# Optimization experiments

Measured on AMD Instinct MI355X. Metric: run time of the kernel, lower is better.

Reference implementation:

```python
import jax, jax.numpy as jnp
import numpy as np

D_MODEL = 1024
NHEADS = 16
DIM_K = D_MODEL // NHEADS


def setup_inputs() -> dict:
    key = jax.random.key(0)
    ks = jax.random.split(key, 7)
    B, S = 4, 2048
    scale = 1.0 / np.sqrt(D_MODEL)
    return {
        "Q": jax.random.normal(ks[0], (B, S, D_MODEL), jnp.float32),
        "K": jax.random.normal(ks[1], (B, S, D_MODEL), jnp.float32),
        "V": jax.random.normal(ks[2], (B, S, D_MODEL), jnp.float32),
        "Wq": jax.random.normal(ks[3], (D_MODEL, D_MODEL), jnp.float32) * scale,
        "Wk": jax.random.normal(ks[4], (D_MODEL, D_MODEL), jnp.float32) * scale,
        "Wv": jax.random.normal(ks[5], (D_MODEL, D_MODEL), jnp.float32) * scale,
        "Wo": jax.random.normal(ks[6], (D_MODEL, D_MODEL), jnp.float32) * scale,
    }


def _split(x):
    # [B,S,D] -> [B,H,S,dk]
    B, S, _ = x.shape
    return x.reshape(B, S, NHEADS, DIM_K).transpose(0, 2, 1, 3)


def reference(Q, K, V, Wq, Wk, Wv, Wo):
    # nn.Linear(x) = x @ W.T; weights stored torch-style [out, in]
    q = _split(Q @ Wq.T)  # [B,H,S,dk]
    k = _split(K @ Wk.T)
    v = _split(V @ Wv.T)
    scores = jnp.einsum("bhsd,bhtd->bhst", q, k) / jnp.sqrt(jnp.float32(DIM_K))
    attn = jax.nn.softmax(scores, axis=-1)
    out = jnp.einsum("bhst,bhtd->bhsd", attn, v)  # [B,H,S,dk]
    B, H, S, dk = out.shape
    out = out.transpose(0, 2, 1, 3).reshape(B, S, H * dk)
    return out @ Wo.T
```

## Files before the change

kernel.cpp:

```cpp
#include <hip/hip_runtime.h>
#include <math.h>
#include <stdint.h>

#define D_MODEL 1024
#define NHEADS  16
#define DK      64
#define BATCH   4
#define SEQ     2048
#define MROWS   (BATCH * SEQ)
#define TENS    ((size_t)MROWS * D_MODEL)
#define WELT    ((size_t)D_MODEL * D_MODEL)

typedef __attribute__((ext_vector_type(8))) _Float16 f16x8;
typedef __attribute__((ext_vector_type(2))) __fp16 h16x2;
typedef __attribute__((ext_vector_type(4))) float f32x4;
typedef __attribute__((ext_vector_type(8))) unsigned short us8;
typedef __attribute__((ext_vector_type(4))) unsigned short us4;

__device__ __forceinline__ unsigned short f2h(float x) {
    _Float16 h = (_Float16)x;
    return __builtin_bit_cast(unsigned short, h);
}

#if __has_builtin(__builtin_amdgcn_exp2f)
__device__ __forceinline__ float fexp2(float x) { return __builtin_amdgcn_exp2f(x); }
#else
__device__ __forceinline__ float fexp2(float x) { return exp2f(x); }
#endif

__device__ __forceinline__ void gld_lds16(const void* g, void* l) {
    __builtin_amdgcn_global_load_lds(
        (__attribute__((address_space(1))) void*)(uintptr_t)(g),
        (__attribute__((address_space(3))) void*)(unsigned)(uintptr_t)(l),
        16, 0, 0);
}

__global__ __launch_bounds__(256)
void convert_kernel(const float* __restrict__ q, const float* __restrict__ k,
                    const float* __restrict__ v, const float* __restrict__ wq,
                    const float* __restrict__ wk, const float* __restrict__ wv,
                    const float* __restrict__ wo, unsigned short* __restrict__ dst)
{
    const int seg = blockIdx.y;
    size_t i = ((size_t)blockIdx.x * 256 + threadIdx.x) * 4;
    const float* src;
    size_t doff, soff;
    if (seg < 3) {
        if (i >= TENS) return;
        src = (seg == 0) ? q : (seg == 1) ? k : v;
        soff = i;
        doff = (size_t)seg * TENS + i;
    } else {
        if (i >= 4 * WELT) return;
        const int widx = (int)(i >> 20);
        src = (widx == 0) ? wq : (widx == 1) ? wk : (widx == 2) ? wv : wo;
        soff = i & (WELT - 1);
        doff = 3 * TENS + i;
    }
    float4 f = *(const float4*)(src + soff);
    us4 o = { f2h(f.x), f2h(f.y), f2h(f.z), f2h(f.w) };
    *(us4*)(dst + doff) = o;
}

__device__ __forceinline__
void gemm_body(const unsigned short* __restrict__ A,
               const unsigned short* __restrict__ B,
               void* __restrict__ C, int N, int K, int omode,
               unsigned short* As, unsigned short* Bs)
{
    const int tid  = threadIdx.x;
    const int wave = tid >> 6;
    const int lane = tid & 63;
    const int g    = lane >> 4;
    const int m15  = lane & 15;
    const int bm   = blockIdx.x * 128;
    const int bn   = blockIdx.y * 128;

    const int srw = lane >> 3;
    const int lc  = (lane & 7) ^ srw;

    const int wr = (wave >> 1) * 64;
    const int wc = (wave & 1) * 64;

    f32x4 acc[4][4];
#pragma unroll
    for (int i = 0; i < 4; ++i)
#pragma unroll
        for (int j = 0; j < 4; ++j) acc[i][j] = (f32x4){0.f, 0.f, 0.f, 0.f};

    for (int k0 = 0; k0 < K; k0 += 64) {
        __syncthreads();
#pragma unroll
        for (int i = 0; i < 4; ++i) {
            const int rb = wave * 32 + i * 8;
            gld_lds16(A + (size_t)(bm + rb + srw) * K + k0 + lc * 8,
                      &As[rb * 64]);
            gld_lds16(B + (size_t)(bn + rb + srw) * K + k0 + lc * 8,
                      &Bs[rb * 64]);
        }
        __syncthreads();

#pragma unroll
        for (int t = 0; t < 2; ++t) {
            f16x8 af[4], bf[4];
#pragma unroll
            for (int i = 0; i < 4; ++i) {
                int row = wr + i * 16 + m15;
                int pc  = (4 * t + g) ^ (row & 7);
                af[i] = *(const f16x8*)&As[row * 64 + pc * 8];
            }
#pragma unroll
            for (int j = 0; j < 4; ++j) {
                int row = wc + j * 16 + m15;
                int pc  = (4 * t + g) ^ (row & 7);
                bf[j] = *(const f16x8*)&Bs[row * 64 + pc * 8];
            }
#pragma unroll
            for (int i = 0; i < 4; ++i)
#pragma unroll
                for (int j = 0; j < 4; ++j)
                    acc[i][j] = __builtin_amdgcn_mfma_f32_16x16x32_f16(
                        af[i], bf[j], acc[i][j], 0, 0, 0);
        }
    }

#pragma unroll
    for (int i = 0; i < 4; ++i) {
        const int gm0 = bm + wr + i * 16 + g * 4;
#pragma unroll
        for (int j = 0; j < 4; ++j) {
            const int gn = bn + wc + j * 16 + m15;
            if (omode == 0) {
#pragma unroll
                for (int r = 0; r < 4; ++r)
                    ((float*)C)[(size_t)(gm0 + r) * N + gn] = acc[i][j][r];
            } else if (omode == 1) {
#pragma unroll
                for (int r = 0; r < 4; ++r)
                    ((unsigned short*)C)[(size_t)(gm0 + r) * N + gn] = f2h(acc[i][j][r]);
            } else {
                const int b_ = gm0 >> 11, s_ = gm0 & 2047;
                const int h_ = gn >> 6,  d_ = gn & 63;
                us4 o = { f2h(acc[i][j][0]), f2h(acc[i][j][1]),
                          f2h(acc[i][j][2]), f2h(acc[i][j][3]) };
                *(us4*)((unsigned short*)C +
                        (((size_t)(b_ * NHEADS + h_) * 256 + (s_ >> 3)) * 64 + d_) * 8
                        + (s_ & 7)) = o;
            }
        }
    }
}

__global__ __launch_bounds__(256)
void proj3_kernel(const unsigned short* __restrict__ qb,
                  const unsigned short* __restrict__ kb,
                  const unsigned short* __restrict__ vb,
                  const unsigned short* __restrict__ wq,
                  const unsigned short* __restrict__ wk,
                  const unsigned short* __restrict__ wv,
                  unsigned short* __restrict__ qproj,
                  unsigned short* __restrict__ kproj,
                  unsigned short* __restrict__ vtw)
{
    __shared__ unsigned short As[128 * 64];
    __shared__ unsigned short Bs[128 * 64];
    const int z = blockIdx.z;
    const unsigned short* A = (z == 0) ? qb : (z == 1) ? kb : vb;
    const unsigned short* B = (z == 0) ? wq : (z == 1) ? wk : wv;
    void* C = (z == 0) ? (void*)qproj : (z == 1) ? (void*)kproj : (void*)vtw;
    gemm_body(A, B, C, D_MODEL, D_MODEL, (z == 2) ? 2 : 1, As, Bs);
}

__global__ __launch_bounds__(256)
void gemm_out_kernel(const unsigned short* __restrict__ A,
                     const unsigned short* __restrict__ B,
                     float* __restrict__ C)
{
    __shared__ unsigned short As[128 * 64];
    __shared__ unsigned short Bs[128 * 64];
    gemm_body(A, B, C, D_MODEL, D_MODEL, 0, As, Bs);
}

__global__ __launch_bounds__(256, 2)
void attn_kernel(const unsigned short* __restrict__ qp,
                 const unsigned short* __restrict__ kp,
                 const unsigned short* __restrict__ vt,
                 unsigned short* __restrict__ ao)
{
    __shared__ unsigned short Ks[2][64 * 64];
    __shared__ unsigned short VTs[2][64 * 64];
    __shared__ unsigned short Ps[4][16 * 72];

    const int tid = threadIdx.x;
    const int w = tid >> 6, lane = tid & 63;
    const int g = lane >> 4, m15 = lane & 15;
    const int qt = blockIdx.x, h = blockIdx.y, b = blockIdx.z;

    const int q0 = qt * 256 + w * 64;
    const size_t rowbase = (size_t)b * SEQ;

    const int srw = lane >> 3;
    const int lc  = (lane & 7) ^ srw;

    const _Float16 qscale = (_Float16)(0.125f * 1.4426950408889634f);
    f16x8 qf[4][2];
#pragma unroll
    for (int mi = 0; mi < 4; ++mi)
#pragma unroll
        for (int t = 0; t < 2; ++t) {
            f16x8 v = *(const f16x8*)(qp + (rowbase + q0 + mi * 16 + m15) * D_MODEL
                                      + h * DK + t * 32 + g * 8);
            qf[mi][t] = v * qscale;
        }

    const _Float16 one16 = (_Float16)1.f;
    const f16x8 onesf = { one16, one16, one16, one16, one16, one16, one16, one16 };

    float mrun[4] = {-INFINITY, -INFINITY, -INFINITY, -INFINITY};
    float lrun[4] = {0.f, 0.f, 0.f, 0.f};

    f32x4 accO[4][4];
#pragma unroll
    for (int mi = 0; mi < 4; ++mi)
#pragma unroll
        for (int i = 0; i < 4; ++i) accO[mi][i] = (f32x4){0.f, 0.f, 0.f, 0.f};

    const unsigned short* kbase = kp + rowbase * D_MODEL + h * DK;
    const unsigned short* vbase = vt + (size_t)(b * NHEADS + h) * DK * SEQ;

    auto stage = [&](int buf, int t) {
#pragma unroll
        for (int it = 0; it < 2; ++it) {
            const int rb = w * 16 + it * 8;
            gld_lds16(kbase + (size_t)(t * 64 + rb + srw) * D_MODEL + lc * 8,
                      &Ks[buf][rb * 64]);
            gld_lds16(vbase + ((size_t)(t * 8 + lc) * 64 + rb + srw) * 8,
                      &VTs[buf][rb * 64]);
        }
    };

    const int NT = SEQ / 64;
    stage(0, 0);
    __syncthreads();

    for (int kt = 0; kt < NT; ++kt) {
        const int cur = kt & 1;
        if (kt + 1 < NT) stage(cur ^ 1, kt + 1);

        f32x4 ST[4][4];
        __builtin_amdgcn_s_setprio(1);
#pragma unroll
        for (int km = 0; km < 4; ++km) {
            const int row = km * 16 + m15;
            f16x8 kf0 = *(const f16x8*)&Ks[cur][row * 64 + ((0 + g) ^ (row & 7)) * 8];
            f16x8 kf1 = *(const f16x8*)&Ks[cur][row * 64 + ((4 + g) ^ (row & 7)) * 8];
#pragma unroll
            for (int mi = 0; mi < 4; ++mi) {
                f32x4 z = (f32x4){0.f, 0.f, 0.f, 0.f};
                z = __builtin_amdgcn_mfma_f32_16x16x32_f16(kf0, qf[mi][0], z, 0, 0, 0);
                z = __builtin_amdgcn_mfma_f32_16x16x32_f16(kf1, qf[mi][1], z, 0, 0, 0);
                ST[km][mi] = z;
            }
        }
        __builtin_amdgcn_s_setprio(0);

        float scl[4];
        f16x8 pf[4][2];
#pragma unroll
        for (int mi = 0; mi < 4; ++mi) {
            float t0 = fmaxf(fmaxf(ST[0][mi][0], ST[0][mi][1]), ST[0][mi][2]);
            float t1 = fmaxf(fmaxf(ST[0][mi][3], ST[1][mi][0]), ST[1][mi][1]);
            float t2 = fmaxf(fmaxf(ST[1][mi][2], ST[1][mi][3]), ST[2][mi][0]);
            float t3 = fmaxf(fmaxf(ST[2][mi][1], ST[2][mi][2]), ST[2][mi][3]);
            float t4 = fmaxf(fmaxf(ST[3][mi][0], ST[3][mi][1]), ST[3][mi][2]);
            float u0 = fmaxf(fmaxf(t0, t1), t2);
            float u1 = fmaxf(fmaxf(t3, t4), ST[3][mi][3]);
            float mx = fmaxf(u0, u1);
            mx = fmaxf(mx, __shfl_xor(mx, 16));
            mx = fmaxf(mx, __shfl_xor(mx, 32));
            float mnew = fmaxf(mrun[mi], mx);
            scl[mi] = fexp2(mrun[mi] - mnew);
            mrun[mi] = mnew;
#pragma unroll
            for (int km = 0; km < 4; ++km) {
                float p0 = fexp2(ST[km][mi][0] - mnew);
                float p1 = fexp2(ST[km][mi][1] - mnew);
                float p2 = fexp2(ST[km][mi][2] - mnew);
                float p3 = fexp2(ST[km][mi][3] - mnew);
                h16x2 d0 = __builtin_amdgcn_cvt_pkrtz(p0, p1);
                h16x2 d1 = __builtin_amdgcn_cvt_pkrtz(p2, p3);
                uint2 wv = { __builtin_bit_cast(unsigned, d0),
                             __builtin_bit_cast(unsigned, d1) };
                *(uint2*)&Ps[w][m15 * 72 + km * 16 + g * 4] = wv;
            }
            pf[mi][0] = *(const f16x8*)&Ps[w][m15 * 72 + g * 8];
            pf[mi][1] = *(const f16x8*)&Ps[w][m15 * 72 + 32 + g * 8];
            f32x4 zs = (f32x4){0.f, 0.f, 0.f, 0.f};
            zs = __builtin_amdgcn_mfma_f32_16x16x32_f16(onesf, pf[mi][0], zs, 0, 0, 0);
            zs = __builtin_amdgcn_mfma_f32_16x16x32_f16(onesf, pf[mi][1], zs, 0, 0, 0);
            lrun[mi] = lrun[mi] * scl[mi] + zs[0];
        }

        int chg = (scl[0] < 1.f) | (scl[1] < 1.f) | (scl[2] < 1.f) | (scl[3] < 1.f);
        if (__any(chg)) {
#pragma unroll
            for (int mi = 0; mi < 4; ++mi)
#pragma unroll
                for (int i = 0; i < 4; ++i) accO[mi][i] *= scl[mi];
        }

        __builtin_amdgcn_s_setprio(1);
#pragma unroll
        for (int i = 0; i < 4; ++i) {
            const int row = i * 16 + m15;
            f16x8 vf0 = *(const f16x8*)&VTs[cur][row * 64 + ((0 + g) ^ (row & 7)) * 8];
            f16x8 vf1 = *(const f16x8*)&VTs[cur][row * 64 + ((4 + g) ^ (row & 7)) * 8];
#pragma unroll
            for (int mi = 0; mi < 4; ++mi) {
                f32x4 a = accO[mi][i];
                a = __builtin_amdgcn_mfma_f32_16x16x32_f16(vf0, pf[mi][0], a, 0, 0, 0);
                a = __builtin_amdgcn_mfma_f32_16x16x32_f16(vf1, pf[mi][1], a, 0, 0, 0);
                accO[mi][i] = a;
            }
        }
        __builtin_amdgcn_s_setprio(0);

        __syncthreads();
    }

#pragma unroll
    for (int mi = 0; mi < 4; ++mi) {
        const float li = 1.f / lrun[mi];
        const size_t qg = rowbase + q0 + mi * 16 + m15;
#pragma unroll
        for (int i = 0; i < 4; ++i) {
            us4 o = { f2h(accO[mi][i][0] * li), f2h(accO[mi][i][1] * li),
                      f2h(accO[mi][i][2] * li), f2h(accO[mi][i][3] * li) };
            *(us4*)(ao + qg * D_MODEL + h * DK + i * 16 + g * 4) = o;
        }
    }
}

extern "C" void kernel_launch(void* const* d_in, const int* in_sizes, int n_in,
                              void* d_out, int out_size, void* d_ws, size_t ws_size,
                              hipStream_t stream)
{
    const float* Q  = (const float*)d_in[0];
    const float* K  = (const float*)d_in[1];
    const float* V  = (const float*)d_in[2];
    const float* Wq = (const float*)d_in[3];
    const float* Wk = (const float*)d_in[4];
    const float* Wv = (const float*)d_in[5];
    const float* Wo = (const float*)d_in[6];

    unsigned short* base = (unsigned short*)d_ws;
    unsigned short* qb = base;
    unsigned short* kb = qb + TENS;
    unsigned short* vb = kb + TENS;
    unsigned short* wq = vb + TENS;
    unsigned short* wk = wq + WELT;
    unsigned short* wv = wk + WELT;
    unsigned short* wo = wv + WELT;
    unsigned short* qproj = wo + WELT;
    unsigned short* kproj = qproj + TENS;
    unsigned short* vtw   = kproj + TENS;
    unsigned short* aow   = vtw + TENS;

    convert_kernel<<<dim3(TENS / 1024, 4), 256, 0, stream>>>(Q, K, V, Wq, Wk, Wv, Wo, base);

    proj3_kernel<<<dim3(MROWS / 128, D_MODEL / 128, 3), 256, 0, stream>>>(
        qb, kb, vb, wq, wk, wv, qproj, kproj, vtw);

    attn_kernel<<<dim3(SEQ / 256, NHEADS, BATCH), 256, 0, stream>>>(
        qproj, kproj, vtw, aow);

    gemm_out_kernel<<<dim3(MROWS / 128, D_MODEL / 128), 256, 0, stream>>>(
        aow, wo, (float*)d_out);
}
```

Baseline: 344.2 us.

## Triple-buffer GEMM LDS loads with 256x128 tiles and 8 waves

The projection and output GEMMs move to 256x128 block tiles with 512 threads and a three-stage LDS ring buffer. Global-to-LDS loads are issued two stages ahead, with explicit vmcnt waits instead of syncthreads around each k-step. MFMA sections are raised in priority via setprio. This aims to hide memory latency and raise per-block reuse, at the cost of much larger LDS use (about 144KB) that limits occupancy to one block per CU.

```diff
diff --git a/kernel.cpp b/kernel.cpp
--- a/kernel.cpp
+++ b/kernel.cpp
@@ -63,17 +63,17 @@
 }
 
 __device__ __forceinline__
-void gemm_body(const unsigned short* __restrict__ A,
-               const unsigned short* __restrict__ B,
-               void* __restrict__ C, int N, int K, int omode,
-               unsigned short* As, unsigned short* Bs)
+void gemm_body8(const unsigned short* __restrict__ A,
+                const unsigned short* __restrict__ B,
+                void* __restrict__ C, int N, int K, int omode,
+                unsigned short* As, unsigned short* Bs)
 {
     const int tid  = threadIdx.x;
     const int wave = tid >> 6;
     const int lane = tid & 63;
     const int g    = lane >> 4;
     const int m15  = lane & 15;
-    const int bm   = blockIdx.x * 128;
+    const int bm   = blockIdx.x * 256;
     const int bn   = blockIdx.y * 128;
 
     const int srw = lane >> 3;
@@ -88,18 +88,25 @@
 #pragma unroll
         for (int j = 0; j < 4; ++j) acc[i][j] = (f32x4){0.f, 0.f, 0.f, 0.f};
 
-    for (int k0 = 0; k0 < K; k0 += 64) {
-        __syncthreads();
+    auto stage = [&](int buf, int t) {
+        const int k0 = t * 64;
 #pragma unroll
         for (int i = 0; i < 4; ++i) {
-            const int rb = wave * 32 + i * 8;
+            const int rb = i * 64 + wave * 8;
             gld_lds16(A + (size_t)(bm + rb + srw) * K + k0 + lc * 8,
-                      &As[rb * 64]);
+                      &As[buf * (256 * 64) + rb * 64]);
+        }
+#pragma unroll
+        for (int j = 0; j < 2; ++j) {
+            const int rb = j * 64 + wave * 8;
             gld_lds16(B + (size_t)(bn + rb + srw) * K + k0 + lc * 8,
-                      &Bs[rb * 64]);
-        }
-        __syncthreads();
-
+                      &Bs[buf * (128 * 64) + rb * 64]);
+        }
+    };
+
+    auto compute = [&](int buf) {
+        const unsigned short* Ab = &As[buf * (256 * 64)];
+        const unsigned short* Bb = &Bs[buf * (128 * 64)];
 #pragma unroll
         for (int t = 0; t < 2; ++t) {
             f16x8 af[4], bf[4];
@@ -107,21 +114,45 @@
             for (int i = 0; i < 4; ++i) {
                 int row = wr + i * 16 + m15;
                 int pc  = (4 * t + g) ^ (row & 7);
-                af[i] = *(const f16x8*)&As[row * 64 + pc * 8];
+                af[i] = *(const f16x8*)&Ab[row * 64 + pc * 8];
             }
 #pragma unroll
             for (int j = 0; j < 4; ++j) {
                 int row = wc + j * 16 + m15;
                 int pc  = (4 * t + g) ^ (row & 7);
-                bf[j] = *(const f16x8*)&Bs[row * 64 + pc * 8];
-            }
+                bf[j] = *(const f16x8*)&Bb[row * 64 + pc * 8];
+            }
+            __builtin_amdgcn_s_setprio(1);
 #pragma unroll
             for (int i = 0; i < 4; ++i)
 #pragma unroll
                 for (int j = 0; j < 4; ++j)
                     acc[i][j] = __builtin_amdgcn_mfma_f32_16x16x32_f16(
                         af[i], bf[j], acc[i][j], 0, 0, 0);
-        }
+            __builtin_amdgcn_s_setprio(0);
+        }
+    };
+
+    const int NT = K / 64;
+    stage(0, 0);
+    stage(1, 1);
+    int cur = 0;
+    for (int t = 0; t < NT; ++t) {
+        if (t + 2 < NT) {
+            int nb = cur + 2; if (nb >= 3) nb -= 3;
+            stage(nb, t + 2);
+            asm volatile("s_waitcnt vmcnt(12)" ::: "memory");
+        } else if (t + 1 < NT) {
+            asm volatile("s_waitcnt vmcnt(6)" ::: "memory");
+        } else {
+            asm volatile("s_waitcnt vmcnt(0)" ::: "memory");
+        }
+        __builtin_amdgcn_s_barrier();
+        __builtin_amdgcn_sched_barrier(0);
+        compute(cur);
+        __builtin_amdgcn_sched_barrier(0);
+        __builtin_amdgcn_s_barrier();
+        ++cur; if (cur == 3) cur = 0;
     }
 
 #pragma unroll
@@ -151,7 +182,7 @@
     }
 }
 
-__global__ __launch_bounds__(256)
+__global__ __launch_bounds__(512)
 void proj3_kernel(const unsigned short* __restrict__ qb,
                   const unsigned short* __restrict__ kb,
                   const unsigned short* __restrict__ vb,
@@ -162,23 +193,23 @@
                   unsigned short* __restrict__ kproj,
                   unsigned short* __restrict__ vtw)
 {
-    __shared__ unsigned short As[128 * 64];
-    __shared__ unsigned short Bs[128 * 64];
+    __shared__ unsigned short As[3 * 256 * 64];
+    __shared__ unsigned short Bs[3 * 128 * 64];
     const int z = blockIdx.z;
     const unsigned short* A = (z == 0) ? qb : (z == 1) ? kb : vb;
     const unsigned short* B = (z == 0) ? wq : (z == 1) ? wk : wv;
     void* C = (z == 0) ? (void*)qproj : (z == 1) ? (void*)kproj : (void*)vtw;
-    gemm_body(A, B, C, D_MODEL, D_MODEL, (z == 2) ? 2 : 1, As, Bs);
-}
-
-__global__ __launch_bounds__(256)
+    gemm_body8(A, B, C, D_MODEL, D_MODEL, (z == 2) ? 2 : 1, As, Bs);
+}
+
+__global__ __launch_bounds__(512)
 void gemm_out_kernel(const unsigned short* __restrict__ A,
                      const unsigned short* __restrict__ B,
                      float* __restrict__ C)
 {
-    __shared__ unsigned short As[128 * 64];
-    __shared__ unsigned short Bs[128 * 64];
-    gemm_body(A, B, C, D_MODEL, D_MODEL, 0, As, Bs);
+    __shared__ unsigned short As[3 * 256 * 64];
+    __shared__ unsigned short Bs[3 * 128 * 64];
+    gemm_body8(A, B, C, D_MODEL, D_MODEL, 0, As, Bs);
 }
 
 __global__ __launch_bounds__(256, 2)
@@ -368,12 +399,12 @@
 
     convert_kernel<<<dim3(TENS / 1024, 4), 256, 0, stream>>>(Q, K, V, Wq, Wk, Wv, Wo, base);
 
-    proj3_kernel<<<dim3(MROWS / 128, D_MODEL / 128, 3), 256, 0, stream>>>(
+    proj3_kernel<<<dim3(MROWS / 256, D_MODEL / 128, 3), 512, 0, stream>>>(
         qb, kb, vb, wq, wk, wv, qproj, kproj, vtw);
 
     attn_kernel<<<dim3(SEQ / 256, NHEADS, BATCH), 256, 0, stream>>>(
         qproj, kproj, vtw, aow);
 
-    gemm_out_kernel<<<dim3(MROWS / 128, D_MODEL / 128), 256, 0, stream>>>(
+    gemm_out_kernel<<<dim3(MROWS / 256, D_MODEL / 128), 512, 0, stream>>>(
         aow, wo, (float*)d_out);
 }
```

After: 329.6 us. 4.2% less time.
